# Optimization experiments

Hardware: AMD Instinct MI355X
Metric: run time of the kernel (lower is better)

Reference implementation:

```python
import jax, jax.numpy as jnp
import numpy as np

B, S, I, H = 64, 2048, 256, 512

def setup_inputs() -> dict:
    key = jax.random.key(0)
    k1, k2, k3, k4 = jax.random.split(key, 4)
    stdv = 1.0 / np.sqrt(H)
    return {
        "x": jax.random.normal(k1, (B, S, I), dtype=jnp.float32),
        "W": jax.random.uniform(k2, (I, 3 * H), dtype=jnp.float32, minval=-stdv, maxval=stdv),
        "U": jax.random.uniform(k3, (H, 3 * H), dtype=jnp.float32, minval=-stdv, maxval=stdv),
        "bias": jax.random.uniform(k4, (3 * H,), dtype=jnp.float32, minval=-stdv, maxval=stdv),
    }

def _lstm_noforget(x, W, U, bias):
    # Precompute input projections for all timesteps: (B, S, 3H)
    x_proj = jnp.einsum("bsi,ig->bsg", x, W) + bias
    h0 = jnp.zeros((x.shape[0], H), dtype=x.dtype)
    c0 = jnp.zeros((x.shape[0], H), dtype=x.dtype)

    def step(carry, xp_t):
        h_t, _ = carry
        gates = xp_t + h_t @ U  # (B, 3H)
        i_t = jax.nn.sigmoid(gates[:, :H])
        g_t = jnp.tanh(gates[:, H:2 * H])
        o_t = jax.nn.sigmoid(gates[:, 2 * H:])
        c_t = i_t * g_t          # no-forget: c does not depend on previous c
        h_t = o_t * jnp.tanh(c_t)
        return (h_t, c_t), h_t

    (h_f, c_f), hs = jax.lax.scan(step, (h0, c0), jnp.swapaxes(x_proj, 0, 1))
    hidden_seq = jnp.swapaxes(hs, 0, 1)  # (B, S, H)
    return hidden_seq, h_f, c_f

def reference(x, W, U, bias):
    return _lstm_noforget(x, W, U, bias)
```

## Files before the change

kernel.cpp:

```cpp
#include <hip/hip_runtime.h>
#include <math.h>

#define B_  64
#define S_  2048
#define I_  256
#define H_  512
#define K_  768
#define G3  1536

#define RT  16
#define JT  4
#define NC  12
#define BLK 192
#define LDA 772

__global__ __launch_bounds__(256) void prep_transpose(
    const float* __restrict__ W,
    const float* __restrict__ U,
    float* __restrict__ Vt)
{
    const int c = blockIdx.y;
    const int k = blockIdx.x * 256 + threadIdx.x;
    if (k < K_) {
        float v = (k < I_) ? W[(size_t)k * G3 + c] : U[(size_t)(k - I_) * G3 + c];
        Vt[(size_t)c * K_ + k] = v;
    }
}

__global__ __launch_bounds__(BLK) void lstm_step(
    const float* __restrict__ x,
    const float* __restrict__ bias,
    const float* __restrict__ Vt,
    const float* __restrict__ h_in,
    float* __restrict__ h_out,
    float* __restrict__ hidden,
    float* __restrict__ hf,
    float* __restrict__ cf,
    int t, int is_last)
{
    __shared__ float Alds[RT * LDA];
    __shared__ float gtile[NC][RT + 1];

    const int tid = threadIdx.x;
    const int rq  = blockIdx.x & 3;
    const int jq  = blockIdx.x >> 2;
    const int r0  = rq * RT;

    for (int f4 = tid; f4 < (RT * I_) / 4; f4 += BLK) {
        const int r  = f4 >> 6;
        const int kk = (f4 & 63) * 4;
        const float4 v = *(const float4*)(x + (size_t)(r0 + r) * (S_ * I_) + (size_t)t * I_ + kk);
        *(float4*)(Alds + r * LDA + kk) = v;
    }
    for (int f4 = tid; f4 < (RT * H_) / 4; f4 += BLK) {
        const int r  = f4 >> 7;
        const int jj = (f4 & 127) * 4;
        const float4 v = *(const float4*)(h_in + (size_t)(r0 + r) * H_ + jj);
        *(float4*)(Alds + r * LDA + I_ + jj) = v;
    }
    __syncthreads();

    const int r      = tid & 15;
    const int c      = tid >> 4;
    const int region = c >> 2;
    const int jl     = c & 3;
    const int j      = jq * JT + jl;
    const int cg     = region * H_ + j;

    const float* __restrict__ wrow = Vt + (size_t)cg * K_;
    const float* __restrict__ arow = Alds + r * LDA;

    float4 acc = make_float4(0.f, 0.f, 0.f, 0.f);
    #pragma unroll 4
    for (int k = 0; k < K_; k += 8) {
        const float4 a0 = *(const float4*)(arow + k);
        const float4 a1 = *(const float4*)(arow + k + 4);
        const float4 w0 = *(const float4*)(wrow + k);
        const float4 w1 = *(const float4*)(wrow + k + 4);
        acc.x += a0.x * w0.x;  acc.y += a0.y * w0.y;
        acc.z += a0.z * w0.z;  acc.w += a0.w * w0.w;
        acc.x += a1.x * w1.x;  acc.y += a1.y * w1.y;
        acc.z += a1.z * w1.z;  acc.w += a1.w * w1.w;
    }
    gtile[c][r] = (acc.x + acc.y) + (acc.z + acc.w) + bias[cg];
    __syncthreads();

    if (tid < RT * JT) {
        const int rr = tid & 15;
        const int jj = tid >> 4;
        const float gi = gtile[0 * JT + jj][rr];
        const float gg = gtile[1 * JT + jj][rr];
        const float go = gtile[2 * JT + jj][rr];
        const float it = 1.f / (1.f + __expf(-gi));
        const float gt = tanhf(gg);
        const float ot = 1.f / (1.f + __expf(-go));
        const float ct = it * gt;
        const float ht = ot * tanhf(ct);
        const int rg = r0 + rr;
        const int jg = jq * JT + jj;
        h_out[(size_t)rg * H_ + jg] = ht;
        hidden[(size_t)rg * (S_ * H_) + (size_t)t * H_ + jg] = ht;
        if (is_last) {
            hf[(size_t)rg * H_ + jg] = ht;
            cf[(size_t)rg * H_ + jg] = ct;
        }
    }
}

extern "C" void kernel_launch(void* const* d_in, const int* in_sizes, int n_in,
                              void* d_out, int out_size, void* d_ws, size_t ws_size,
                              hipStream_t stream) {
    const float* x    = (const float*)d_in[0];
    const float* W    = (const float*)d_in[1];
    const float* U    = (const float*)d_in[2];
    const float* bias = (const float*)d_in[3];

    float* out    = (float*)d_out;
    float* hidden = out;
    float* hf     = out + (size_t)B_ * S_ * H_;
    float* cf     = hf + (size_t)B_ * H_;

    float* Vt = (float*)d_ws;
    float* h0 = Vt + (size_t)G3 * K_;
    float* h1 = h0 + (size_t)B_ * H_;

    hipLaunchKernelGGL(prep_transpose, dim3(3, G3), dim3(256), 0, stream, W, U, Vt);
    hipMemsetAsync(h0, 0, (size_t)B_ * H_ * sizeof(float), stream);

    float* hin = h0;
    float* hout = h1;
    for (int t = 0; t < S_; ++t) {
        hipLaunchKernelGGL(lstm_step, dim3(512), dim3(BLK), 0, stream,
                           x, bias, Vt, hin, hout, hidden, hf, cf, t, (t == S_ - 1) ? 1 : 0);
        float* tmp = hin; hin = hout; hout = tmp;
    }
}
```

Baseline: 32.98 ms.

## Replace per-timestep launches with persistent cooperative kernel and grid barrier

Replaces 2048 separate step launches with one cooperative persistent kernel of 256 blocks. Each block keeps its slice of the weights resident in LDS, computes a 16x24 gate tile with a split-K register-tiled dot product reduced through DPP and shuffles, and prefetches the next timestep's x while other threads apply the activations. Timesteps are separated by a flag-based grid barrier in global memory instead of kernel boundaries, which removes launch overhead and repeated weight reloads. The barrier has a spin budget that could break out early and allow a race, and it relies on every block being co-resident.

```diff
diff --git a/kernel.cpp b/kernel.cpp
--- a/kernel.cpp
+++ b/kernel.cpp
@@ -1,18 +1,25 @@
 #include <hip/hip_runtime.h>
 #include <math.h>
 
-#define B_  64
-#define S_  2048
-#define I_  256
-#define H_  512
-#define K_  768
-#define G3  1536
-
-#define RT  16
-#define JT  4
-#define NC  12
-#define BLK 192
-#define LDA 772
+#define B_   64
+#define S_   2048
+#define I_   256
+#define H_   512
+#define K_   768
+#define G3   1536
+
+#define NBLK 256
+#define NTHR 384
+#define ROWS 16
+#define COLS 24
+#define HC   8
+#define LDA  772
+
+#define W_OFF 0
+#define A_OFF (COLS * LDA)
+#define G_OFF (A_OFF + ROWS * LDA)
+#define SMEM_FLOATS (G_OFF + 3 * ROWS * HC)
+#define SMEM_BYTES  (SMEM_FLOATS * 4)
 
 __global__ __launch_bounds__(256) void prep_transpose(
     const float* __restrict__ W,
@@ -27,89 +34,184 @@
     }
 }
 
-__global__ __launch_bounds__(BLK) void lstm_step(
+template <int CTRL>
+__device__ __forceinline__ float dpp_add(float v) {
+    int r = __builtin_amdgcn_update_dpp(0, __float_as_int(v), CTRL, 0xF, 0xF, false);
+    return v + __int_as_float(r);
+}
+
+__global__ __launch_bounds__(NTHR, 2) void lstm_persist(
     const float* __restrict__ x,
     const float* __restrict__ bias,
     const float* __restrict__ Vt,
-    const float* __restrict__ h_in,
-    float* __restrict__ h_out,
+    float* __restrict__ h0,
+    float* __restrict__ h1,
     float* __restrict__ hidden,
     float* __restrict__ hf,
     float* __restrict__ cf,
-    int t, int is_last)
+    unsigned* __restrict__ flags,
+    unsigned* __restrict__ gen)
 {
-    __shared__ float Alds[RT * LDA];
-    __shared__ float gtile[NC][RT + 1];
+    extern __shared__ float smem[];
+    float* Wlds = smem + W_OFF;
+    float* Alds = smem + A_OFF;
+    float* gt   = smem + G_OFF;
 
     const int tid = threadIdx.x;
-    const int rq  = blockIdx.x & 3;
-    const int jq  = blockIdx.x >> 2;
-    const int r0  = rq * RT;
-
-    for (int f4 = tid; f4 < (RT * I_) / 4; f4 += BLK) {
-        const int r  = f4 >> 6;
-        const int kk = (f4 & 63) * 4;
-        const float4 v = *(const float4*)(x + (size_t)(r0 + r) * (S_ * I_) + (size_t)t * I_ + kk);
-        *(float4*)(Alds + r * LDA + kk) = v;
-    }
-    for (int f4 = tid; f4 < (RT * H_) / 4; f4 += BLK) {
-        const int r  = f4 >> 7;
-        const int jj = (f4 & 127) * 4;
-        const float4 v = *(const float4*)(h_in + (size_t)(r0 + r) * H_ + jj);
-        *(float4*)(Alds + r * LDA + I_ + jj) = v;
-    }
-    __syncthreads();
-
-    const int r      = tid & 15;
-    const int c      = tid >> 4;
-    const int region = c >> 2;
-    const int jl     = c & 3;
-    const int j      = jq * JT + jl;
-    const int cg     = region * H_ + j;
-
-    const float* __restrict__ wrow = Vt + (size_t)cg * K_;
-    const float* __restrict__ arow = Alds + r * LDA;
-
-    float4 acc = make_float4(0.f, 0.f, 0.f, 0.f);
-    #pragma unroll 4
-    for (int k = 0; k < K_; k += 8) {
-        const float4 a0 = *(const float4*)(arow + k);
-        const float4 a1 = *(const float4*)(arow + k + 4);
-        const float4 w0 = *(const float4*)(wrow + k);
-        const float4 w1 = *(const float4*)(wrow + k + 4);
-        acc.x += a0.x * w0.x;  acc.y += a0.y * w0.y;
-        acc.z += a0.z * w0.z;  acc.w += a0.w * w0.w;
-        acc.x += a1.x * w1.x;  acc.y += a1.y * w1.y;
-        acc.z += a1.z * w1.z;  acc.w += a1.w * w1.w;
-    }
-    gtile[c][r] = (acc.x + acc.y) + (acc.z + acc.w) + bias[cg];
-    __syncthreads();
-
-    if (tid < RT * JT) {
-        const int rr = tid & 15;
-        const int jj = tid >> 4;
-        const float gi = gtile[0 * JT + jj][rr];
-        const float gg = gtile[1 * JT + jj][rr];
-        const float go = gtile[2 * JT + jj][rr];
-        const float it = 1.f / (1.f + __expf(-gi));
-        const float gt = tanhf(gg);
-        const float ot = 1.f / (1.f + __expf(-go));
-        const float ct = it * gt;
-        const float ht = ot * tanhf(ct);
-        const int rg = r0 + rr;
-        const int jg = jq * JT + jj;
-        h_out[(size_t)rg * H_ + jg] = ht;
-        hidden[(size_t)rg * (S_ * H_) + (size_t)t * H_ + jg] = ht;
-        if (is_last) {
-            hf[(size_t)rg * H_ + jg] = ht;
-            cf[(size_t)rg * H_ + jg] = ct;
-        }
+    const int bid = blockIdx.x;
+    const int rg  = bid & 3;
+    const int cgp = bid >> 2;
+    const int r0  = rg * ROWS;
+    const int j0  = cgp * HC;
+
+    for (int f4 = tid; f4 < COLS * (K_ / 4); f4 += NTHR) {
+        const int cc  = f4 / (K_ / 4);
+        const int kf4 = f4 % (K_ / 4);
+        const int region = cc >> 3;
+        const int cl  = cc & 7;
+        const float4 v = *(const float4*)(Vt + (size_t)(region * H_ + j0 + cl) * K_ + kf4 * 4);
+        *(float4*)(Wlds + cc * LDA + kf4 * 4) = v;
+    }
+    for (int f4 = tid; f4 < ROWS * (I_ / 4); f4 += NTHR) {
+        const int r = f4 >> 6, kf4 = f4 & 63;
+        const float4 v = *(const float4*)(x + (size_t)(r0 + r) * ((size_t)S_ * I_) + kf4 * 4);
+        *(float4*)(Alds + r * LDA + kf4 * 4) = v;
+    }
+
+    const int ks   = tid & 31;
+    const int tile = tid >> 5;
+    const int tr   = tile / 6;
+    const int tc   = tile % 6;
+    const int rw0  = tr * 8;
+
+    float bi = 0.f, bg = 0.f, bo = 0.f;
+    if (tid < ROWS * HC) {
+        const int cl = tid & 7;
+        bi = bias[0 * H_ + j0 + cl];
+        bg = bias[1 * H_ + j0 + cl];
+        bo = bias[2 * H_ + j0 + cl];
+    }
+
+    float* hprev = h0;
+    float* hnext = h1;
+    unsigned budget = 2000000u;
+
+    #pragma unroll 1
+    for (int t = 0; t < S_; ++t) {
+        for (int f4 = tid; f4 < ROWS * (H_ / 4); f4 += NTHR) {
+            const int r = f4 >> 7, jf4 = f4 & 127;
+            const float4 v = *(const float4*)(hprev + (size_t)(r0 + r) * H_ + jf4 * 4);
+            *(float4*)(Alds + r * LDA + I_ + jf4 * 4) = v;
+        }
+        __syncthreads();
+
+        float acc[8][4];
+        #pragma unroll
+        for (int i = 0; i < 8; ++i) { acc[i][0] = 0.f; acc[i][1] = 0.f; acc[i][2] = 0.f; acc[i][3] = 0.f; }
+
+        #pragma unroll
+        for (int j = 0; j < 6; ++j) {
+            const int kk = ks * 4 + j * 128;
+            const float4 w0 = *(const float4*)(Wlds + (tc * 4 + 0) * LDA + kk);
+            const float4 w1 = *(const float4*)(Wlds + (tc * 4 + 1) * LDA + kk);
+            const float4 w2 = *(const float4*)(Wlds + (tc * 4 + 2) * LDA + kk);
+            const float4 w3 = *(const float4*)(Wlds + (tc * 4 + 3) * LDA + kk);
+            #pragma unroll
+            for (int i = 0; i < 8; ++i) {
+                const float4 a = *(const float4*)(Alds + (rw0 + i) * LDA + kk);
+                acc[i][0] += a.x * w0.x + a.y * w0.y + a.z * w0.z + a.w * w0.w;
+                acc[i][1] += a.x * w1.x + a.y * w1.y + a.z * w1.z + a.w * w1.w;
+                acc[i][2] += a.x * w2.x + a.y * w2.y + a.z * w2.z + a.w * w2.w;
+                acc[i][3] += a.x * w3.x + a.y * w3.y + a.z * w3.z + a.w * w3.w;
+            }
+        }
+
+        #pragma unroll
+        for (int i = 0; i < 8; ++i) {
+            #pragma unroll
+            for (int c = 0; c < 4; ++c) {
+                float v = acc[i][c];
+                v = dpp_add<0x121>(v);
+                v = dpp_add<0x122>(v);
+                v = dpp_add<0x124>(v);
+                v = dpp_add<0x128>(v);
+                v += __shfl_xor(v, 16, 32);
+                acc[i][c] = v;
+            }
+        }
+        if (ks == 0) {
+            const int region = tc >> 1;
+            const int cl0 = (tc & 1) * 4;
+            #pragma unroll
+            for (int i = 0; i < 8; ++i) {
+                *(float4*)(gt + region * (ROWS * HC) + (rw0 + i) * HC + cl0) =
+                    make_float4(acc[i][0], acc[i][1], acc[i][2], acc[i][3]);
+            }
+        }
+        __syncthreads();
+
+        if (tid < ROWS * HC) {
+            const int r = tid >> 3, cl = tid & 7;
+            const float gi = gt[0 * (ROWS * HC) + tid] + bi;
+            const float gg = gt[1 * (ROWS * HC) + tid] + bg;
+            const float go = gt[2 * (ROWS * HC) + tid] + bo;
+            const float it = 1.f / (1.f + __expf(-gi));
+            const float g2 = tanhf(gg);
+            const float ot = 1.f / (1.f + __expf(-go));
+            const float ct = it * g2;
+            const float ht = ot * tanhf(ct);
+            const int rr = r0 + r, jj = j0 + cl;
+            hnext[(size_t)rr * H_ + jj] = ht;
+            hidden[(size_t)rr * ((size_t)S_ * H_) + (size_t)t * H_ + jj] = ht;
+            if (t == S_ - 1) {
+                hf[(size_t)rr * H_ + jj] = ht;
+                cf[(size_t)rr * H_ + jj] = ct;
+            }
+        } else if (t + 1 < S_) {
+            for (int f4 = tid - 128; f4 < ROWS * (I_ / 4); f4 += (NTHR - 128)) {
+                const int r = f4 >> 6, kf4 = f4 & 63;
+                const float4 v = *(const float4*)(x + (size_t)(r0 + r) * ((size_t)S_ * I_)
+                                                  + (size_t)(t + 1) * I_ + kf4 * 4);
+                *(float4*)(Alds + r * LDA + kf4 * 4) = v;
+            }
+        }
+
+        __syncthreads();
+        const unsigned target = (unsigned)(t + 1);
+        if (tid == 0) {
+            __threadfence();
+            __hip_atomic_store(flags + bid, target, __ATOMIC_RELAXED, __HIP_MEMORY_SCOPE_AGENT);
+        }
+        if (bid == 0) {
+            for (int i = tid; i < NBLK; i += NTHR) {
+                while (__hip_atomic_load(flags + i, __ATOMIC_RELAXED, __HIP_MEMORY_SCOPE_AGENT) < target) {
+                    if (budget == 0) break;
+                    --budget;
+                }
+            }
+            __syncthreads();
+            if (tid == 0) {
+                __threadfence();
+                __hip_atomic_store(gen, target, __ATOMIC_RELAXED, __HIP_MEMORY_SCOPE_AGENT);
+            }
+        }
+        if (tid == 0) {
+            while (__hip_atomic_load(gen, __ATOMIC_RELAXED, __HIP_MEMORY_SCOPE_AGENT) < target) {
+                if (budget == 0) break;
+                --budget;
+            }
+            __threadfence();
+        }
+        __syncthreads();
+
+        float* tmp = hprev; hprev = hnext; hnext = tmp;
     }
 }
 
 extern "C" void kernel_launch(void* const* d_in, const int* in_sizes, int n_in,
                               void* d_out, int out_size, void* d_ws, size_t ws_size,
                               hipStream_t stream) {
+    (void)in_sizes; (void)n_in; (void)out_size; (void)ws_size;
     const float* x    = (const float*)d_in[0];
     const float* W    = (const float*)d_in[1];
     const float* U    = (const float*)d_in[2];
@@ -123,15 +225,22 @@
     float* Vt = (float*)d_ws;
     float* h0 = Vt + (size_t)G3 * K_;
     float* h1 = h0 + (size_t)B_ * H_;
+    unsigned* flags = (unsigned*)(h1 + (size_t)B_ * H_);
+    unsigned* gen   = flags + 320;
 
     hipLaunchKernelGGL(prep_transpose, dim3(3, G3), dim3(256), 0, stream, W, U, Vt);
     hipMemsetAsync(h0, 0, (size_t)B_ * H_ * sizeof(float), stream);
-
-    float* hin = h0;
-    float* hout = h1;
-    for (int t = 0; t < S_; ++t) {
-        hipLaunchKernelGGL(lstm_step, dim3(512), dim3(BLK), 0, stream,
-                           x, bias, Vt, hin, hout, hidden, hf, cf, t, (t == S_ - 1) ? 1 : 0);
-        float* tmp = hin; hin = hout; hout = tmp;
-    }
-}
+    hipMemsetAsync(flags, 0, 384 * sizeof(unsigned), stream);
+
+    static int attr_set = 0;
+    if (!attr_set) {
+        hipFuncSetAttribute((const void*)lstm_persist,
+                            hipFuncAttributeMaxDynamicSharedMemorySize, SMEM_BYTES);
+        attr_set = 1;
+    }
+
+    void* args[] = { (void*)&x, (void*)&bias, (void*)&Vt, (void*)&h0, (void*)&h1,
+                     (void*)&hidden, (void*)&hf, (void*)&cf, (void*)&flags, (void*)&gen };
+    hipLaunchCooperativeKernel((const void*)lstm_persist, dim3(NBLK), dim3(NTHR),
+                               args, SMEM_BYTES, stream);
+}
```

Measured after the change: 39.04 ms. 18.4% more time.
